# Kernel optimization log

Hardware: AMD Instinct MI355X
Metric: run time of the kernel (lower is better)

## Reference

```python
import jax, jax.numpy as jnp
import numpy as np

B, D, K, A, P = 4096, 512, 128, 32, 16  # batch, theta dim, mixture comps, alpha dim, hutchinson probes


def setup_inputs() -> dict:
    key = jax.random.key(0)
    k1, k2, k3, k4 = jax.random.split(key, 4)
    thetas = jax.random.normal(k1, (B, D), dtype=jnp.float32)
    alpha = jax.random.normal(k2, (K, A), dtype=jnp.float32)
    W = jax.random.normal(k3, (A, D), dtype=jnp.float32) / jnp.sqrt(jnp.float32(A))
    v_int = jax.random.randint(k4, (P, B, D), 0, 2, dtype=jnp.int32)  # -> Rademacher via 2v-1
    return {"thetas": thetas, "alpha": alpha, "W": W, "v_int": v_int,
            "N_dataset": 100000, "K_alpha_samples": K}


def _log_density(thetas, alpha, W, N_dataset, K_alpha):
    # Tempered Gaussian mixture: mu_k = alpha_k @ W;
    # logp_b = (N/(N+1)) * (logsumexp_k -0.5||theta_b - mu_k||^2 - log K)
    mu = alpha @ W                                        # [K, D]
    # ||t - mu||^2 expanded to avoid a [B,K,D] intermediate
    sq = (jnp.sum(thetas * thetas, -1, keepdims=True)
          - 2.0 * thetas @ mu.T
          + jnp.sum(mu * mu, -1)[None, :])                # [B, K]
    temper = jnp.float32(N_dataset) / (jnp.float32(N_dataset) + 1.0)
    return temper * (jax.nn.logsumexp(-0.5 * sq, axis=1) - jnp.log(jnp.float32(K_alpha)))


def reference(thetas, alpha, W, v_int, N_dataset, K_alpha_samples):
    v = (2 * v_int - 1).astype(thetas.dtype)              # [P, B, D] Rademacher

    def logp_sum(t):
        return jnp.sum(_log_density(t, alpha, W, N_dataset, K_alpha_samples))

    score = jax.grad(logp_sum)                            # gradiente wrt thetas
    g = score(thetas)                                     # [B, D]

    # Hutchinson trace of the per-sample Hessian via forward-over-reverse HVPs,
    # batched over probes (fuses the torch per-probe autograd.grad loop).
    def hvp(vi):
        return jax.jvp(score, (thetas,), (vi,))[1]        # [B, D]

    Hv = jax.vmap(hvp)(v)                                 # [P, B, D]
    traces = jnp.mean(jnp.sum(v * Hv, axis=-1), axis=0)   # [B]

    loss = 0.5 * jnp.sum(g * g, axis=-1) + traces         # [B]
    return jnp.mean(loss)
```

## Files before the change

kernel.cpp:

```cpp
#include <hip/hip_runtime.h>
#include <hip/hip_bf16.h>
#include <stdint.h>

#define Bsz 4096
#define Dn  512
#define Kn  128
#define Pn  16
#define An  32
#define TB  16

typedef __attribute__((ext_vector_type(4))) float  floatx4;
typedef __attribute__((ext_vector_type(8))) short  shortx8;

__device__ __forceinline__ unsigned short f2bf(float x) {
    union { float f; uint32_t u; } v; v.f = x;
    uint32_t u = v.u;
    uint32_t r = (u + 0x7FFFu + ((u >> 16) & 1u)) >> 16;
    return (unsigned short)r;
}

__global__ __launch_bounds__(256) void k_mu(const float* __restrict__ alpha,
                                            const float* __restrict__ W,
                                            unsigned short* __restrict__ mu_bf,
                                            float* __restrict__ munorm,
                                            float* __restrict__ out) {
    __shared__ float al[An];
    __shared__ float red[4];
    int k = blockIdx.x, t = threadIdx.x;
    if (k == 0 && t == 0) *out = 0.f;
    if (t < An) al[t] = alpha[k * An + t];
    __syncthreads();
    int d0 = t, d1 = t + 256;
    float a0 = 0.f, a1 = 0.f;
#pragma unroll
    for (int a = 0; a < An; ++a) {
        float av = al[a];
        a0 = fmaf(av, W[a * Dn + d0], a0);
        a1 = fmaf(av, W[a * Dn + d1], a1);
    }
    mu_bf[k * Dn + d0] = f2bf(a0);  mu_bf[k * Dn + d1] = f2bf(a1);
    float nrm = a0 * a0 + a1 * a1;
#pragma unroll
    for (int msk = 1; msk < 64; msk <<= 1) nrm += __shfl_xor(nrm, msk);
    if ((t & 63) == 0) red[t >> 6] = nrm;
    __syncthreads();
    if (t == 0) munorm[k] = red[0] + red[1] + red[2] + red[3];
}

__global__ __launch_bounds__(512) void k_gram(const unsigned short* __restrict__ mu_bf,
                                              unsigned short* __restrict__ G_bf) {
    __shared__ short at[TB][520];
    const int tid = threadIdx.x;
    const int lane = tid & 63;
    const int wv = tid >> 6;
    const int m = lane & 15;
    const int q = lane >> 4;
    const int i0 = blockIdx.x * TB;

    const int r = tid >> 5, c0 = (tid & 31) * 16;
    const int4* src = (const int4*)(mu_bf + (size_t)(i0 + r) * Dn + c0);
    *(int4*)&at[r][c0]     = src[0];
    *(int4*)&at[r][c0 + 8] = src[1];

    const int kcol = wv * 16 + m;
    shortx8 bfrag[16];
    const unsigned short* mb = mu_bf + (size_t)kcol * Dn + q * 8;
#pragma unroll
    for (int dc = 0; dc < 16; ++dc) bfrag[dc] = *(const shortx8*)(mb + dc * 32);
    __syncthreads();

    floatx4 acc = {0.f, 0.f, 0.f, 0.f};
#pragma unroll
    for (int dc = 0; dc < 16; ++dc) {
        shortx8 a = *(const shortx8*)&at[m][dc * 32 + q * 8];
        acc = __builtin_amdgcn_mfma_f32_16x16x32_bf16(a, bfrag[dc], acc, 0, 0, 0);
    }
#pragma unroll
    for (int i = 0; i < 4; ++i)
        G_bf[(size_t)(i0 + q * 4 + i) * Kn + kcol] = f2bf(acc[i]);
}

__global__ __launch_bounds__(512, 4) void k_main(
    const float* __restrict__ thetas,
    const int* __restrict__ v_int,
    const unsigned short* __restrict__ mu_bf,
    const float* __restrict__ munorm,
    const unsigned short* __restrict__ G_bf,
    const int* __restrict__ Np,
    float* __restrict__ out)
{
    __shared__ short vt[2][TB][520];
    __shared__ float S_l[TB][132];
    __shared__ float w_l[TB][132];
    __shared__ short wbf[TB][136];
    __shared__ float part[2][8][TB][2];
    __shared__ float thn[TB];
    __shared__ float SwS[TB];

    const int tid = threadIdx.x;
    const int lane = tid & 63;
    const int wv = tid >> 6;
    const int m = lane & 15;
    const int q = lane >> 4;

    const int tileb = blockIdx.x >> 1;
    const int phalf = blockIdx.x & 1;
    const int b0 = tileb * TB;
    const int p0 = phalf * 8;

    const float Nf = (float)(*Np);
    const float temper = Nf / (Nf + 1.0f);

    const int kcol = wv * 16 + m;
    shortx8 mufrag[16];
    {
        const unsigned short* mb = mu_bf + (size_t)kcol * Dn + q * 8;
#pragma unroll
        for (int dc = 0; dc < 16; ++dc)
            mufrag[dc] = *(const shortx8*)(mb + dc * 32);
    }

    const int r = tid >> 5;
    const int c0 = (tid & 31) * 16;
    const size_t PB = (size_t)Bsz * Dn;
    const int* vrow = v_int + (size_t)(b0 + r) * Dn + c0;

    int4 buf[4];
    {
        const int4* g = (const int4*)(vrow + (size_t)p0 * PB);
#pragma unroll
        for (int j = 0; j < 4; ++j) buf[j] = g[j];
    }
    {
        const float4* tg = (const float4*)(thetas + (size_t)(b0 + r) * Dn + c0);
        float tn = 0.f;
#pragma unroll
        for (int j = 0; j < 4; ++j) {
            float4 f = tg[j];
            tn += f.x * f.x + f.y * f.y + f.z * f.z + f.w * f.w;
            short4 h;
            h.x = (short)f2bf(f.x); h.y = (short)f2bf(f.y);
            h.z = (short)f2bf(f.z); h.w = (short)f2bf(f.w);
            *(short4*)&vt[0][r][c0 + j * 4] = h;
        }
#pragma unroll
        for (int msk = 1; msk < 32; msk <<= 1) tn += __shfl_xor(tn, msk);
        if ((tid & 31) == 0) thn[r] = tn;
    }
    __syncthreads();

    {
        floatx4 acc = {0.f, 0.f, 0.f, 0.f};
#pragma unroll
        for (int dc = 0; dc < 16; ++dc) {
            shortx8 a = *(const shortx8*)&vt[0][m][dc * 32 + q * 8];
            acc = __builtin_amdgcn_mfma_f32_16x16x32_bf16(a, mufrag[dc], acc, 0, 0, 0);
        }
#pragma unroll
        for (int i = 0; i < 4; ++i) S_l[q * 4 + i][kcol] = acc[i];
    }
    __syncthreads();

    {
        const int b = tid >> 5, s = tid & 31;
        float l[4];
        float mx = -3.4e38f;
        float tnb = thn[b];
#pragma unroll
        for (int j = 0; j < 4; ++j) {
            int k = s + 32 * j;
            l[j] = -0.5f * (tnb - 2.f * S_l[b][k] + munorm[k]);
            mx = fmaxf(mx, l[j]);
        }
#pragma unroll
        for (int msk = 1; msk < 32; msk <<= 1) mx = fmaxf(mx, __shfl_xor(mx, msk));
        float se = 0.f, ses = 0.f;
        float e[4];
#pragma unroll
        for (int j = 0; j < 4; ++j) {
            int k = s + 32 * j;
            e[j] = __expf(l[j] - mx);
            se += e[j];
            ses += e[j] * S_l[b][k];
        }
#pragma unroll
        for (int msk = 1; msk < 32; msk <<= 1) { se += __shfl_xor(se, msk); ses += __shfl_xor(ses, msk); }
        float inv = 1.f / se;
#pragma unroll
        for (int j = 0; j < 4; ++j) {
            int k = s + 32 * j;
            float wvv = e[j] * inv;
            w_l[b][k] = wvv;
            wbf[b][k] = (short)f2bf(wvv);
        }
        if (s == 0) SwS[b] = ses * inv;
    }
    __syncthreads();

    {
        shortx8 gfrag[4];
        const unsigned short* gb = G_bf + (size_t)kcol * Kn + q * 8;
#pragma unroll
        for (int kc = 0; kc < 4; ++kc) gfrag[kc] = *(const shortx8*)(gb + kc * 32);
        floatx4 acc = {0.f, 0.f, 0.f, 0.f};
#pragma unroll
        for (int kc = 0; kc < 4; ++kc) {
            shortx8 a = *(const shortx8*)&wbf[m][kc * 32 + q * 8];
            acc = __builtin_amdgcn_mfma_f32_16x16x32_bf16(a, gfrag[kc], acc, 0, 0, 0);
        }
        float sg[4];
#pragma unroll
        for (int i = 0; i < 4; ++i) sg[i] = w_l[q * 4 + i][kcol] * acc[i];
#pragma unroll
        for (int msk = 1; msk < 16; msk <<= 1) {
#pragma unroll
            for (int i = 0; i < 4; ++i) sg[i] += __shfl_xor(sg[i], msk);
        }
        if (m == 0) {
#pragma unroll
            for (int i = 0; i < 4; ++i) part[0][wv][q * 4 + i][0] = sg[i];
        }
    }
    __syncthreads();

    float lossA = 0.f, tracc = 0.f;
    if (tid < TB) {
        float wGw = 0.f;
#pragma unroll
        for (int w8 = 0; w8 < 8; ++w8) wGw += part[0][w8][tid][0];
        if (phalf == 0)
            lossA = 0.5f * temper * temper * (wGw - 2.f * SwS[tid] + thn[tid])
                    - temper * (float)Dn;
    }

#pragma unroll
    for (int p = 0; p < 8; ++p) {
#pragma unroll
        for (int j = 0; j < 4; ++j) {
            int4 w4 = buf[j];
            short4 h;
            h.x = (short)(0x3F80 | ((w4.x ^ 1) << 15));
            h.y = (short)(0x3F80 | ((w4.y ^ 1) << 15));
            h.z = (short)(0x3F80 | ((w4.z ^ 1) << 15));
            h.w = (short)(0x3F80 | ((w4.w ^ 1) << 15));
            *(short4*)&vt[p & 1][r][c0 + j * 4] = h;
        }
        __syncthreads();
        if (p < 7) {
            const int4* g = (const int4*)(vrow + (size_t)(p0 + p + 1) * PB);
#pragma unroll
            for (int j = 0; j < 4; ++j) buf[j] = g[j];
        }
        if (p > 0 && tid < TB) {
            float S1 = 0.f, S2 = 0.f;
#pragma unroll
            for (int w8 = 0; w8 < 8; ++w8) {
                S1 += part[(p - 1) & 1][w8][tid][0];
                S2 += part[(p - 1) & 1][w8][tid][1];
            }
            tracc += S1 - S2 * S2;
        }
        floatx4 acc = {0.f, 0.f, 0.f, 0.f};
#pragma unroll
        for (int dc = 0; dc < 16; ++dc) {
            shortx8 a = *(const shortx8*)&vt[p & 1][m][dc * 32 + q * 8];
            acc = __builtin_amdgcn_mfma_f32_16x16x32_bf16(a, mufrag[dc], acc, 0, 0, 0);
        }
        float s1[4], s2[4];
#pragma unroll
        for (int i = 0; i < 4; ++i) {
            float T = acc[i];
            float wt = w_l[q * 4 + i][kcol];
            s1[i] = wt * T * T;
            s2[i] = wt * T;
        }
#pragma unroll
        for (int msk = 1; msk < 16; msk <<= 1) {
#pragma unroll
            for (int i = 0; i < 4; ++i) {
                s1[i] += __shfl_xor(s1[i], msk);
                s2[i] += __shfl_xor(s2[i], msk);
            }
        }
        if (m == 0) {
#pragma unroll
            for (int i = 0; i < 4; ++i) {
                part[p & 1][wv][q * 4 + i][0] = s1[i];
                part[p & 1][wv][q * 4 + i][1] = s2[i];
            }
        }
    }
    __syncthreads();
    if (tid < TB) {
        float S1 = 0.f, S2 = 0.f;
#pragma unroll
        for (int w8 = 0; w8 < 8; ++w8) {
            S1 += part[1][w8][tid][0];
            S2 += part[1][w8][tid][1];
        }
        tracc += S1 - S2 * S2;
        float res = temper * tracc * (1.0f / (float)Pn) + lossA;
#pragma unroll
        for (int msk = 1; msk < 16; msk <<= 1) res += __shfl_xor(res, msk);
        if (tid == 0) atomicAdd(out, res * (1.0f / (float)Bsz));
    }
}

extern "C" void kernel_launch(void* const* d_in, const int* in_sizes, int n_in,
                              void* d_out, int out_size, void* d_ws, size_t ws_size,
                              hipStream_t stream) {
    const float* thetas = (const float*)d_in[0];
    const float* alpha  = (const float*)d_in[1];
    const float* W      = (const float*)d_in[2];
    const int*   v_int  = (const int*)d_in[3];
    const int*   Np     = (const int*)d_in[4];

    char* ws = (char*)d_ws;
    unsigned short* mu_bf  = (unsigned short*)ws;
    float*          munorm = (float*)(ws + 131072);
    unsigned short* G_bf   = (unsigned short*)(ws + 131072 + 1024);

    float* out = (float*)d_out;
    k_mu  <<<dim3(Kn), dim3(256), 0, stream>>>(alpha, W, mu_bf, munorm, out);
    k_gram<<<dim3(8),  dim3(512), 0, stream>>>(mu_bf, G_bf);
    k_main<<<dim3(512), dim3(512), 0, stream>>>(thetas, v_int, mu_bf, munorm, G_bf, Np, out);
}
```

Baseline: 216.3 us.

## Replace Gram-matrix kernel with direct ||w·mu||² via transposed mu

Removes the separate k_gram launch that formed G = mu·muᵀ. Instead, k_mu also writes a transposed bf16 copy of mu, and k_main computes w·mu with MFMA over 512 columns, summing the squares to get wᵀGw. This drops one kernel launch and its dependency, at the cost of more MFMA work and global reads of mu_t inside the main kernel. It also packs the Rademacher bf16 conversion into two 32-bit XOR words per four values.

```diff
diff --git a/kernel.cpp b/kernel.cpp
--- a/kernel.cpp
+++ b/kernel.cpp
@@ -22,6 +22,7 @@
 __global__ __launch_bounds__(256) void k_mu(const float* __restrict__ alpha,
                                             const float* __restrict__ W,
                                             unsigned short* __restrict__ mu_bf,
+                                            unsigned short* __restrict__ mu_t,
                                             float* __restrict__ munorm,
                                             float* __restrict__ out) {
     __shared__ float al[An];
@@ -38,46 +39,15 @@
         a0 = fmaf(av, W[a * Dn + d0], a0);
         a1 = fmaf(av, W[a * Dn + d1], a1);
     }
-    mu_bf[k * Dn + d0] = f2bf(a0);  mu_bf[k * Dn + d1] = f2bf(a1);
+    unsigned short h0 = f2bf(a0), h1 = f2bf(a1);
+    mu_bf[k * Dn + d0] = h0;  mu_bf[k * Dn + d1] = h1;
+    mu_t[d0 * Kn + k] = h0;   mu_t[d1 * Kn + k] = h1;
     float nrm = a0 * a0 + a1 * a1;
 #pragma unroll
     for (int msk = 1; msk < 64; msk <<= 1) nrm += __shfl_xor(nrm, msk);
     if ((t & 63) == 0) red[t >> 6] = nrm;
     __syncthreads();
     if (t == 0) munorm[k] = red[0] + red[1] + red[2] + red[3];
-}
-
-__global__ __launch_bounds__(512) void k_gram(const unsigned short* __restrict__ mu_bf,
-                                              unsigned short* __restrict__ G_bf) {
-    __shared__ short at[TB][520];
-    const int tid = threadIdx.x;
-    const int lane = tid & 63;
-    const int wv = tid >> 6;
-    const int m = lane & 15;
-    const int q = lane >> 4;
-    const int i0 = blockIdx.x * TB;
-
-    const int r = tid >> 5, c0 = (tid & 31) * 16;
-    const int4* src = (const int4*)(mu_bf + (size_t)(i0 + r) * Dn + c0);
-    *(int4*)&at[r][c0]     = src[0];
-    *(int4*)&at[r][c0 + 8] = src[1];
-
-    const int kcol = wv * 16 + m;
-    shortx8 bfrag[16];
-    const unsigned short* mb = mu_bf + (size_t)kcol * Dn + q * 8;
-#pragma unroll
-    for (int dc = 0; dc < 16; ++dc) bfrag[dc] = *(const shortx8*)(mb + dc * 32);
-    __syncthreads();
-
-    floatx4 acc = {0.f, 0.f, 0.f, 0.f};
-#pragma unroll
-    for (int dc = 0; dc < 16; ++dc) {
-        shortx8 a = *(const shortx8*)&at[m][dc * 32 + q * 8];
-        acc = __builtin_amdgcn_mfma_f32_16x16x32_bf16(a, bfrag[dc], acc, 0, 0, 0);
-    }
-#pragma unroll
-    for (int i = 0; i < 4; ++i)
-        G_bf[(size_t)(i0 + q * 4 + i) * Kn + kcol] = f2bf(acc[i]);
 }
 
 __global__ __launch_bounds__(512, 4) void k_main(
@@ -85,7 +55,7 @@
     const int* __restrict__ v_int,
     const unsigned short* __restrict__ mu_bf,
     const float* __restrict__ munorm,
-    const unsigned short* __restrict__ G_bf,
+    const unsigned short* __restrict__ mu_t,
     const int* __restrict__ Np,
     float* __restrict__ out)
 {
@@ -198,19 +168,20 @@
     __syncthreads();
 
     {
-        shortx8 gfrag[4];
-        const unsigned short* gb = G_bf + (size_t)kcol * Kn + q * 8;
-#pragma unroll
-        for (int kc = 0; kc < 4; ++kc) gfrag[kc] = *(const shortx8*)(gb + kc * 32);
-        floatx4 acc = {0.f, 0.f, 0.f, 0.f};
-#pragma unroll
-        for (int kc = 0; kc < 4; ++kc) {
-            shortx8 a = *(const shortx8*)&wbf[m][kc * 32 + q * 8];
-            acc = __builtin_amdgcn_mfma_f32_16x16x32_bf16(a, gfrag[kc], acc, 0, 0, 0);
-        }
-        float sg[4];
-#pragma unroll
-        for (int i = 0; i < 4; ++i) sg[i] = w_l[q * 4 + i][kcol] * acc[i];
+        float sg[4] = {0.f, 0.f, 0.f, 0.f};
+#pragma unroll
+        for (int ct = 0; ct < 4; ++ct) {
+            const unsigned short* mt = mu_t + (size_t)(wv * 64 + ct * 16 + m) * Kn + q * 8;
+            floatx4 acc = {0.f, 0.f, 0.f, 0.f};
+#pragma unroll
+            for (int kc = 0; kc < 4; ++kc) {
+                shortx8 a = *(const shortx8*)&wbf[m][kc * 32 + q * 8];
+                shortx8 bfr = *(const shortx8*)(mt + kc * 32);
+                acc = __builtin_amdgcn_mfma_f32_16x16x32_bf16(a, bfr, acc, 0, 0, 0);
+            }
+#pragma unroll
+            for (int i = 0; i < 4; ++i) sg[i] += acc[i] * acc[i];
+        }
 #pragma unroll
         for (int msk = 1; msk < 16; msk <<= 1) {
 #pragma unroll
@@ -238,12 +209,10 @@
 #pragma unroll
         for (int j = 0; j < 4; ++j) {
             int4 w4 = buf[j];
-            short4 h;
-            h.x = (short)(0x3F80 | ((w4.x ^ 1) << 15));
-            h.y = (short)(0x3F80 | ((w4.y ^ 1) << 15));
-            h.z = (short)(0x3F80 | ((w4.z ^ 1) << 15));
-            h.w = (short)(0x3F80 | ((w4.w ^ 1) << 15));
-            *(short4*)&vt[p & 1][r][c0 + j * 4] = h;
+            uint32_t lo = 0xBF80BF80u ^ ((uint32_t)w4.x << 15) ^ ((uint32_t)w4.y << 31);
+            uint32_t hi = 0xBF80BF80u ^ ((uint32_t)w4.z << 15) ^ ((uint32_t)w4.w << 31);
+            uint2 pk; pk.x = lo; pk.y = hi;
+            *(uint2*)&vt[p & 1][r][c0 + j * 4] = pk;
         }
         __syncthreads();
         if (p < 7) {
@@ -318,10 +287,9 @@
     char* ws = (char*)d_ws;
     unsigned short* mu_bf  = (unsigned short*)ws;
     float*          munorm = (float*)(ws + 131072);
-    unsigned short* G_bf   = (unsigned short*)(ws + 131072 + 1024);
+    unsigned short* mu_t   = (unsigned short*)(ws + 131072 + 1024);
 
     float* out = (float*)d_out;
-    k_mu  <<<dim3(Kn), dim3(256), 0, stream>>>(alpha, W, mu_bf, munorm, out);
-    k_gram<<<dim3(8),  dim3(512), 0, stream>>>(mu_bf, G_bf);
-    k_main<<<dim3(512), dim3(512), 0, stream>>>(thetas, v_int, mu_bf, munorm, G_bf, Np, out);
-}
+    k_mu  <<<dim3(Kn),  dim3(256), 0, stream>>>(alpha, W, mu_bf, mu_t, munorm, out);
+    k_main<<<dim3(512), dim3(512), 0, stream>>>(thetas, v_int, mu_bf, munorm, mu_t, Np, out);
+}
```

New measurement: 218.2 us. No clear change (+0.9%).
